# Performance work log

Measured on AMD Instinct MI355X. Metric: run time of the kernel, lower is better.

The kernel has to match this reference:

```python
import jax, jax.numpy as jnp
import numpy as np

DN = ('NCHW', 'OIHW', 'NCHW')

def conv(x, w, b=None, stride=1, pad=0):
    y = jax.lax.conv_general_dilated(x, w, (stride, stride), [(pad, pad), (pad, pad)],
                                     dimension_numbers=DN)
    return y if b is None else y + b[None, :, None, None]

def conv_t(x, w, b, stride=2, pad=1):
    # PyTorch ConvTranspose2d: w is (in, out, kh, kw); equivalent to an
    # input-dilated conv with spatially flipped, in/out-swapped kernel.
    k = w.shape[2]
    w2 = jnp.flip(w, (2, 3)).transpose(1, 0, 2, 3)
    p = k - 1 - pad
    y = jax.lax.conv_general_dilated(x, w2, (1, 1), [(p, p), (p, p)],
                                     lhs_dilation=(stride, stride), dimension_numbers=DN)
    return y + b[None, :, None, None]

def res_block(x, wa, wb):
    h = conv(jax.nn.relu(x), wa, None, 1, 1)   # 3x3, no bias
    h = conv(jax.nn.relu(h), wb, None, 1, 0)   # 1x1, no bias
    return x + h

def vq(x, codebook):
    B, C, H, W = x.shape
    xf = x.transpose(0, 2, 3, 1).reshape(-1, C)                      # (N, D)
    d = ((xf * xf).sum(-1, keepdims=True)
         - 2.0 * xf @ codebook.T
         + (codebook * codebook).sum(-1)[None, :])
    idx = jnp.argmin(d, axis=1)                                      # (N,)
    q = jnp.take(codebook, idx, axis=0)                              # gather (N, D)
    return q.reshape(B, H, W, C).transpose(0, 3, 1, 2)

def setup_inputs() -> dict:
    key = jax.random.key(0)
    ks = jax.random.split(key, 16)
    r = lambda i, shape: jax.random.normal(ks[i], shape, jnp.float32) * 0.05
    K, D = 512, 64
    return {
        'x': jax.random.normal(ks[0], (32, 1, 256, 256), jnp.float32),
        'w_e1': r(1, (32, 1, 4, 4)),   'b_e1': jnp.zeros((32,), jnp.float32),
        'w_e2': r(2, (64, 32, 4, 4)),  'b_e2': jnp.zeros((64,), jnp.float32),
        'w_er1a': r(3, (32, 64, 3, 3)), 'w_er1b': r(4, (64, 32, 1, 1)),
        'w_er2a': r(5, (32, 64, 3, 3)), 'w_er2b': r(6, (64, 32, 1, 1)),
        'w_pre': r(7, (D, 64, 1, 1)),  'b_pre': jnp.zeros((D,), jnp.float32),
        'codebook': jax.random.uniform(ks[8], (K, D), jnp.float32, -1.0 / K, 1.0 / K),
        'w_d1': r(9, (64, D, 3, 3)),   'b_d1': jnp.zeros((64,), jnp.float32),
        'w_dr1a': r(10, (32, 64, 3, 3)), 'w_dr1b': r(11, (64, 32, 1, 1)),
        'w_dr2a': r(12, (32, 64, 3, 3)), 'w_dr2b': r(13, (64, 32, 1, 1)),
        'w_t1': r(14, (64, 32, 4, 4)), 'b_t1': jnp.zeros((32,), jnp.float32),
        'w_t2': r(15, (32, 1, 4, 4)),  'b_t2': jnp.zeros((1,), jnp.float32),
    }

def reference(x, w_e1, b_e1, w_e2, b_e2, w_er1a, w_er1b, w_er2a, w_er2b,
              w_pre, b_pre, codebook, w_d1, b_d1, w_dr1a, w_dr1b,
              w_dr2a, w_dr2b, w_t1, b_t1, w_t2, b_t2):
    # Encoder
    h = jax.nn.relu(conv(x, w_e1, b_e1, 2, 1))     # (B,32,128,128)
    h = conv(h, w_e2, b_e2, 2, 1)                  # (B,64,64,64)
    h = res_block(h, w_er1a, w_er1b)
    h = res_block(h, w_er2a, w_er2b)
    # pre-VQ 1x1 conv
    h = conv(h, w_pre, b_pre, 1, 0)                # (B,64,64,64)
    # Vector quantization
    q = vq(h, codebook)
    # Decoder
    d = conv(q, w_d1, b_d1, 1, 1)
    d = res_block(d, w_dr1a, w_dr1b)
    d = res_block(d, w_dr2a, w_dr2b)
    d = jax.nn.relu(conv_t(d, w_t1, b_t1))         # (B,32,128,128)
    d = conv_t(d, w_t2, b_t2)                      # (B,1,256,256)
    return d
```

## Files before the change

kernel.cpp:

```cpp
#include <hip/hip_runtime.h>
#include <hip/hip_bf16.h>


__device__ __forceinline__ float rp_elem(const float* __restrict__ src,
                                         int i, int COUT, int CIN, int KK)
{
    const int co = i % COUT;
    const int t  = i / COUT;
    const int kk = t % KK;
    const int ci = t / KK;
    return src[(co * CIN + ci) * KK + kk];
}

__global__ __launch_bounds__(256) void repack_all(
    const float* __restrict__ e1,  const float* __restrict__ e2,
    const float* __restrict__ er1a, const float* __restrict__ er1b,
    const float* __restrict__ er2a, const float* __restrict__ er2b,
    const float* __restrict__ pre, const float* __restrict__ d1,
    const float* __restrict__ dr1a, const float* __restrict__ dr1b,
    const float* __restrict__ dr2a, const float* __restrict__ dr2b,
    const float* __restrict__ t1, const float* __restrict__ cb,
    float* __restrict__ WR)
{
    const int idx = blockIdx.x * 256 + threadIdx.x;
    if (idx >= 221696) return;
    float v;
    if      (idx < 512)    v = rp_elem(e1,   idx,          32,  1, 16);
    else if (idx < 33280)  v = rp_elem(e2,   idx - 512,    64, 32, 16);
    else if (idx < 51712)  v = rp_elem(er1a, idx - 33280,  32, 64,  9);
    else if (idx < 53760)  v = rp_elem(er1b, idx - 51712,  64, 32,  1);
    else if (idx < 72192)  v = rp_elem(er2a, idx - 53760,  32, 64,  9);
    else if (idx < 74240)  v = rp_elem(er2b, idx - 72192,  64, 32,  1);
    else if (idx < 78336)  v = rp_elem(pre,  idx - 74240,  64, 64,  1);
    else if (idx < 115200) v = rp_elem(d1,   idx - 78336,  64, 64,  9);
    else if (idx < 133632) v = rp_elem(dr1a, idx - 115200, 32, 64,  9);
    else if (idx < 135680) v = rp_elem(dr1b, idx - 133632, 64, 32,  1);
    else if (idx < 154112) v = rp_elem(dr2a, idx - 135680, 32, 64,  9);
    else if (idx < 156160) v = rp_elem(dr2b, idx - 154112, 64, 32,  1);
    else if (idx < 188928) {
        const int i  = idx - 156160;
        const int co = i & 31;
        const int q  = (i >> 5) & 3;
        const int k2 = (i >> 7) & 127;
        const int pr = i >> 14;
        const int pc = q >> 1, tb = q & 1;
        const int ci = k2 >> 1, ta = k2 & 1;
        const int kh = (1 - pr) + 2 * ta, kw = (1 - pc) + 2 * tb;
        v = t1[((ci * 32 + co) * 4 + kh) * 4 + kw];
    } else {
        const int i = idx - 188928;
        const int code = i & 511;
        const int dim  = i >> 9;
        v = cb[code * 64 + dim];
    }
    WR[idx] = v;
}

__global__ __launch_bounds__(256) void vq_prep_ee(
    const float* __restrict__ cb, float* __restrict__ ee)
{
    const int k = blockIdx.x * 256 + threadIdx.x;
    const float* __restrict__ cp = cb + (size_t)k * 64;
    float s = 0.0f;
#pragma unroll
    for (int i = 0; i < 64; i++) s = fmaf(cp[i], cp[i], s);
    ee[k] = s;
}

template<int CTOT, int CPB, int CIN, int K, int S, int PAD,
         bool RELU_IN, bool HAS_BIAS, bool RESID, bool RELU_OUT>
__global__ __launch_bounds__(256) void conv_gemm(
    const float* __restrict__ in, const float* __restrict__ wr,
    const float* __restrict__ bias, const float* __restrict__ resid,
    float* __restrict__ out,
    int H, int W, int OH, int OW)
{
    constexpr int KK  = K * K;
    constexpr int CIC = (K == 1) ? 8 : 1;
    constexpr int TS  = (K == 4) ? 2 : 1;
    constexpr int KC  = CIC * KK / TS;
    constexpr int NCH = (CIN * TS) / CIC;
    constexpr int NT  = 256;
    constexpr int CPTHD = CPB / 4;
    __shared__ __align__(16) float As[2][KC * NT];

    const int tid = threadIdx.x;
    const int tpx = tid & 63;
    const int tco = __builtin_amdgcn_readfirstlane(tid >> 6);
    const int co0 = blockIdx.y * CPB + tco * CPTHD;

    const int ohow = OH * OW;
    const int n_st = blockIdx.x * NT + tid;
    const int b_st = n_st / ohow;
    const int hw_s = n_st % ohow;
    const int ih0 = (hw_s / OW) * S - PAD;
    const int iw0 = (hw_s % OW) * S - PAD;
    const float* __restrict__ inb = in + (size_t)b_st * CIN * H * W;

    float acc[CPTHD][4];
#pragma unroll
    for (int c = 0; c < CPTHD; c++) {
        const float bz = HAS_BIAS ? bias[co0 + c] : 0.0f;
#pragma unroll
        for (int q = 0; q < 4; q++) acc[c][q] = bz;
    }

    float pf[KC];
    auto stage_load = [&](int ch) {
#pragma unroll
        for (int t = 0; t < KC; t++) {
            int ci, kh, kw;
            if constexpr (K == 1) {
                ci = ch * 8 + t; kh = 0; kw = 0;
            } else if constexpr (K == 3) {
                ci = ch; kh = t / 3; kw = t % 3;
            } else {
                ci = ch >> 1;
                const int kk = ((ch & 1) << 3) + t;
                kh = kk >> 2; kw = kk & 3;
            }
            const int ih = ih0 + kh, iw = iw0 + kw;
            float v = 0.0f;
            if (ih >= 0 && ih < H && iw >= 0 && iw < W)
                v = inb[(size_t)ci * H * W + ih * W + iw];
            if (RELU_IN) v = fmaxf(v, 0.0f);
            pf[t] = v;
        }
    };

    stage_load(0);
#pragma unroll
    for (int t = 0; t < KC; t++) As[0][t * NT + tid] = pf[t];
    __syncthreads();

#pragma unroll 2
    for (int c = 0; c < NCH; c++) {
        const int cur = c & 1;
        if (c + 1 < NCH) stage_load(c + 1);

#pragma unroll
        for (int t = 0; t < KC; t++) {
            const float4 a4 = *(const float4*)(As[cur] + t * NT + tpx * 4);
            const float* __restrict__ wk =
                wr + (size_t)(c * KC + t) * CTOT + co0;
#pragma unroll
            for (int cc = 0; cc < CPTHD; cc++) {
                const float w = wk[cc];
                acc[cc][0] = fmaf(a4.x, w, acc[cc][0]);
                acc[cc][1] = fmaf(a4.y, w, acc[cc][1]);
                acc[cc][2] = fmaf(a4.z, w, acc[cc][2]);
                acc[cc][3] = fmaf(a4.w, w, acc[cc][3]);
            }
        }

        if (c + 1 < NCH) {
#pragma unroll
            for (int t = 0; t < KC; t++) As[1 - cur][t * NT + tid] = pf[t];
        }
        __syncthreads();
    }

    const int n_c  = blockIdx.x * NT + tpx * 4;
    const int b_c  = n_c / ohow;
    const int hw_c = n_c % ohow;
    float* __restrict__ op = out + (size_t)b_c * CTOT * ohow + hw_c;
    const float* __restrict__ rp =
        RESID ? (resid + (size_t)b_c * CTOT * ohow + hw_c) : nullptr;
#pragma unroll
    for (int c = 0; c < CPTHD; c++) {
        const size_t off = (size_t)(co0 + c) * ohow;
        float4 r = make_float4(acc[c][0], acc[c][1], acc[c][2], acc[c][3]);
        if (RESID) {
            const float4 rv = *(const float4*)(rp + off);
            r.x += rv.x; r.y += rv.y; r.z += rv.z; r.w += rv.w;
        }
        if (RELU_OUT) {
            r.x = fmaxf(r.x, 0.f); r.y = fmaxf(r.y, 0.f);
            r.z = fmaxf(r.z, 0.f); r.w = fmaxf(r.w, 0.f);
        }
        *(float4*)(op + off) = r;
    }
}

__global__ __launch_bounds__(512, 4) void res_tile(
    const float* __restrict__ in, const float* __restrict__ wr1,
    const float* __restrict__ wr2, float* __restrict__ out)
{
    __shared__ __align__(16) float S[13824];

    const int tid = threadIdx.x;
    const int p   = tid & 127;
    const int cog = __builtin_amdgcn_readfirstlane(tid >> 7);
    const int a   = p >> 5;
    const int c0  = (p & 31) * 2;

    const int n0   = blockIdx.x * 256;
    const int b    = n0 >> 12;
    const int row0 = (n0 & 4095) >> 6;
    const float* __restrict__ inb = in + (size_t)b * 64 * 4096;

    float4 pf4[7];
    auto stage_issue = [&](int half) {
#pragma unroll
        for (int m = 0; m < 7; m++) {
            const int f4 = m * 512 + tid;
            float4 v = make_float4(0.f, 0.f, 0.f, 0.f);
            if (f4 < 3456) {
                const int ci  = f4 / 108;
                const int rem = f4 - ci * 108;
                const int r6  = rem / 18;
                const int c4  = rem - r6 * 18;
                const int ih  = row0 + r6 - 1;
                if (ih >= 0 && ih < 64 && c4 >= 1 && c4 <= 16)
                    v = *(const float4*)(inb + (size_t)(half * 32 + ci) * 4096
                                         + ih * 64 + (c4 * 4 - 4));
            }
            pf4[m] = v;
        }
    };
    auto stage_commit = [&]() {
#pragma unroll
        for (int m = 0; m < 7; m++) {
            const int f4 = m * 512 + tid;
            if (f4 < 3456) {
                float4 v = pf4[m];
                v.x = fmaxf(v.x, 0.f); v.y = fmaxf(v.y, 0.f);
                v.z = fmaxf(v.z, 0.f); v.w = fmaxf(v.w, 0.f);
                *(float4*)(S + f4 * 4) = v;
            }
        }
    };

    const int co1 = cog * 8;
    float acc1[8][2];
#pragma unroll
    for (int c = 0; c < 8; c++) { acc1[c][0] = 0.0f; acc1[c][1] = 0.0f; }

    auto conv1_half = [&](int h) {
#pragma unroll 2
        for (int c = 0; c < 32; c++) {
            const float* __restrict__ wb =
                wr1 + (size_t)((h * 32 + c) * 9) * 32 + co1;
#pragma unroll
            for (int kh = 0; kh < 3; kh++) {
                const float* __restrict__ tp =
                    S + c * 432 + (a + kh) * 72 + 4 + c0;
                const float2 L = *(const float2*)(tp - 2);
                const float2 M = *(const float2*)(tp);
                const float2 R = *(const float2*)(tp + 2);
                const float xm = L.y;
                const float x0 = M.x;
                const float x1 = M.y;
                const float x2 = R.x;
                const float* __restrict__ wk = wb + (size_t)(kh * 3) * 32;
#pragma unroll
                for (int cc = 0; cc < 8; cc++) {
                    const float w = wk[cc];
                    acc1[cc][0] = fmaf(xm, w, acc1[cc][0]);
                    acc1[cc][1] = fmaf(x0, w, acc1[cc][1]);
                }
#pragma unroll
                for (int cc = 0; cc < 8; cc++) {
                    const float w = wk[32 + cc];
                    acc1[cc][0] = fmaf(x0, w, acc1[cc][0]);
                    acc1[cc][1] = fmaf(x1, w, acc1[cc][1]);
                }
#pragma unroll
                for (int cc = 0; cc < 8; cc++) {
                    const float w = wk[64 + cc];
                    acc1[cc][0] = fmaf(x1, w, acc1[cc][0]);
                    acc1[cc][1] = fmaf(x2, w, acc1[cc][1]);
                }
            }
        }
    };

    stage_issue(0);
    stage_commit();
    __syncthreads();
    stage_issue(1);
    conv1_half(0);
    __syncthreads();
    stage_commit();
    __syncthreads();
    conv1_half(1);
    __syncthreads();

#pragma unroll
    for (int cc = 0; cc < 8; cc++)
        *(float2*)(S + (co1 + cc) * 256 + p * 2) =
            make_float2(acc1[cc][0], acc1[cc][1]);
    __syncthreads();

    const int co2 = cog * 16;
    float acc2[16][2];
#pragma unroll
    for (int c = 0; c < 16; c++) { acc2[c][0] = 0.0f; acc2[c][1] = 0.0f; }

#pragma unroll 4
    for (int k = 0; k < 32; k++) {
        float2 m2 = *(const float2*)(S + k * 256 + p * 2);
        m2.x = fmaxf(m2.x, 0.f);
        m2.y = fmaxf(m2.y, 0.f);
        const float* __restrict__ wk = wr2 + (size_t)k * 64 + co2;
#pragma unroll
        for (int cc = 0; cc < 16; cc++) {
            const float w = wk[cc];
            acc2[cc][0] = fmaf(m2.x, w, acc2[cc][0]);
            acc2[cc][1] = fmaf(m2.y, w, acc2[cc][1]);
        }
    }

    const int hw = (n0 & 4095) + p * 2;
    const float* __restrict__ rp = inb + hw;
    float* __restrict__ op = out + (size_t)b * 64 * 4096 + hw;
#pragma unroll
    for (int cc = 0; cc < 16; cc++) {
        const size_t off = (size_t)(co2 + cc) * 4096;
        const float2 rv = *(const float2*)(rp + off);
        *(float2*)(op + off) =
            make_float2(acc2[cc][0] + rv.x, acc2[cc][1] + rv.y);
    }
}

__global__ __launch_bounds__(512, 4) void conv3_tile(
    const float* __restrict__ in, const float* __restrict__ wr,
    const float* __restrict__ bias, float* __restrict__ out)
{
    __shared__ __align__(16) float S[13824];

    const int tid = threadIdx.x;
    const int p   = tid & 127;
    const int cog = __builtin_amdgcn_readfirstlane(tid >> 7);
    const int a   = p >> 5;
    const int c0  = (p & 31) * 2;

    const int n0   = blockIdx.x * 256;
    const int b    = n0 >> 12;
    const int row0 = (n0 & 4095) >> 6;
    const float* __restrict__ inb = in + (size_t)b * 64 * 4096;

    float4 pf4[7];
    auto stage_issue = [&](int half) {
#pragma unroll
        for (int m = 0; m < 7; m++) {
            const int f4 = m * 512 + tid;
            float4 v = make_float4(0.f, 0.f, 0.f, 0.f);
            if (f4 < 3456) {
                const int ci  = f4 / 108;
                const int rem = f4 - ci * 108;
                const int r6  = rem / 18;
                const int c4  = rem - r6 * 18;
                const int ih  = row0 + r6 - 1;
                if (ih >= 0 && ih < 64 && c4 >= 1 && c4 <= 16)
                    v = *(const float4*)(inb + (size_t)(half * 32 + ci) * 4096
                                         + ih * 64 + (c4 * 4 - 4));
            }
            pf4[m] = v;
        }
    };
    auto stage_commit = [&]() {
#pragma unroll
        for (int m = 0; m < 7; m++) {
            const int f4 = m * 512 + tid;
            if (f4 < 3456) *(float4*)(S + f4 * 4) = pf4[m];
        }
    };

    const int co1 = cog * 16;
    float acc[16][2];
#pragma unroll
    for (int cc = 0; cc < 16; cc++) {
        const float bz = bias[co1 + cc];
        acc[cc][0] = bz; acc[cc][1] = bz;
    }

    auto conv_half = [&](int h) {
#pragma unroll 2
        for (int c = 0; c < 32; c++) {
            const float* __restrict__ wb =
                wr + (size_t)((h * 32 + c) * 9) * 64 + co1;
#pragma unroll
            for (int kh = 0; kh < 3; kh++) {
                const float* __restrict__ tp =
                    S + c * 432 + (a + kh) * 72 + 4 + c0;
                const float2 L = *(const float2*)(tp - 2);
                const float2 M = *(const float2*)(tp);
                const float2 R = *(const float2*)(tp + 2);
                const float xm = L.y;
                const float x0 = M.x;
                const float x1 = M.y;
                const float x2 = R.x;
                const float* __restrict__ wk = wb + (size_t)(kh * 3) * 64;
#pragma unroll
                for (int cc = 0; cc < 16; cc++) {
                    const float w = wk[cc];
                    acc[cc][0] = fmaf(xm, w, acc[cc][0]);
                    acc[cc][1] = fmaf(x0, w, acc[cc][1]);
                }
#pragma unroll
                for (int cc = 0; cc < 16; cc++) {
                    const float w = wk[64 + cc];
                    acc[cc][0] = fmaf(x0, w, acc[cc][0]);
                    acc[cc][1] = fmaf(x1, w, acc[cc][1]);
                }
#pragma unroll
                for (int cc = 0; cc < 16; cc++) {
                    const float w = wk[128 + cc];
                    acc[cc][0] = fmaf(x1, w, acc[cc][0]);
                    acc[cc][1] = fmaf(x2, w, acc[cc][1]);
                }
            }
        }
    };

    stage_issue(0);
    stage_commit();
    __syncthreads();
    stage_issue(1);
    conv_half(0);
    __syncthreads();
    stage_commit();
    __syncthreads();
    conv_half(1);

    const int hw = (n0 & 4095) + p * 2;
    float* __restrict__ op = out + (size_t)b * 64 * 4096 + hw;
#pragma unroll
    for (int cc = 0; cc < 16; cc++)
        *(float2*)(op + (size_t)(co1 + cc) * 4096) =
            make_float2(acc[cc][0], acc[cc][1]);
}

__global__ __launch_bounds__(512, 4) void conv4s2_tile(
    const float* __restrict__ in, const float* __restrict__ wr,
    const float* __restrict__ bias, float* __restrict__ out)
{
    __shared__ __align__(16) float S[13056];

    const int tid = threadIdx.x;
    const int p   = tid & 63;
    const int cog = __builtin_amdgcn_readfirstlane(tid >> 6);
    const int a   = p >> 5;
    const int c0  = (p & 31) * 2;

    const int n0   = blockIdx.x * 128;
    const int b    = n0 >> 12;
    const int row0 = (n0 & 4095) >> 6;
    const float* __restrict__ inb = in + (size_t)b * 32 * 16384;

    float4 pf4[7];
    auto stage_issue = [&](int half) {
#pragma unroll
        for (int m = 0; m < 7; m++) {
            const int f4 = m * 512 + tid;
            float4 v = make_float4(0.f, 0.f, 0.f, 0.f);
            if (f4 < 3264) {
                const int ci  = f4 / 204;
                const int rem = f4 - ci * 204;
                const int r6  = rem / 34;
                const int s   = rem - r6 * 34;
                const int ih  = 2 * row0 - 1 + r6;
                if (ih >= 0 && ih < 128 && s >= 1 && s <= 32)
                    v = *(const float4*)(inb + (size_t)(half * 16 + ci) * 16384
                                         + ih * 128 + (s - 1) * 4);
            }
            pf4[m] = v;
        }
    };
    auto stage_commit = [&]() {
#pragma unroll
        for (int m = 0; m < 7; m++) {
            const int f4 = m * 512 + tid;
            if (f4 < 3264) *(float4*)(S + f4 * 4) = pf4[m];
        }
    };

    const int co1 = cog * 8;
    float acc[8][2];
#pragma unroll
    for (int cc = 0; cc < 8; cc++) {
        const float bz = bias[co1 + cc];
        acc[cc][0] = bz; acc[cc][1] = bz;
    }

    auto conv_half = [&](int h) {
#pragma unroll 2
        for (int c = 0; c < 16; c++) {
            const float* __restrict__ wb =
                wr + (size_t)((h * 16 + c) * 16) * 64 + co1;
#pragma unroll
            for (int kh = 0; kh < 4; kh++) {
                const float* __restrict__ base =
                    S + c * 816 + (2 * a + kh) * 136 + 2 * c0;
                const float4 Q = *(const float4*)(base + 4);
                const float x0 = base[3];
                const float x5 = base[8];
                const float x1 = Q.x, x2 = Q.y, x3 = Q.z, x4 = Q.w;
                const float* __restrict__ wk = wb + (size_t)(kh * 4) * 64;
#pragma unroll
                for (int cc = 0; cc < 8; cc++) {
                    const float w = wk[cc];
                    acc[cc][0] = fmaf(x0, w, acc[cc][0]);
                    acc[cc][1] = fmaf(x2, w, acc[cc][1]);
                }
#pragma unroll
                for (int cc = 0; cc < 8; cc++) {
                    const float w = wk[64 + cc];
                    acc[cc][0] = fmaf(x1, w, acc[cc][0]);
                    acc[cc][1] = fmaf(x3, w, acc[cc][1]);
                }
#pragma unroll
                for (int cc = 0; cc < 8; cc++) {
                    const float w = wk[128 + cc];
                    acc[cc][0] = fmaf(x2, w, acc[cc][0]);
                    acc[cc][1] = fmaf(x4, w, acc[cc][1]);
                }
#pragma unroll
                for (int cc = 0; cc < 8; cc++) {
                    const float w = wk[192 + cc];
                    acc[cc][0] = fmaf(x3, w, acc[cc][0]);
                    acc[cc][1] = fmaf(x5, w, acc[cc][1]);
                }
            }
        }
    };

    stage_issue(0);
    stage_commit();
    __syncthreads();
    stage_issue(1);
    conv_half(0);
    __syncthreads();
    stage_commit();
    __syncthreads();
    conv_half(1);

    const int hw = (n0 & 4095) + p * 2;
    float* __restrict__ op = out + (size_t)b * 64 * 4096 + hw;
#pragma unroll
    for (int cc = 0; cc < 8; cc++)
        *(float2*)(op + (size_t)(co1 + cc) * 4096) =
            make_float2(acc[cc][0], acc[cc][1]);
}

__global__ __launch_bounds__(512, 4) void conv1x1_tile(
    const float* __restrict__ in, const float* __restrict__ wr,
    const float* __restrict__ bias, float* __restrict__ out)
{
    __shared__ __align__(16) float S[8192];

    const int tid = threadIdx.x;
    const int p   = tid & 127;
    const int cog = __builtin_amdgcn_readfirstlane(tid >> 7);

    const int n0  = blockIdx.x * 256;
    const int b   = n0 >> 12;
    const int hw0 = n0 & 4095;
    const float* __restrict__ inb = in + (size_t)b * 64 * 4096 + hw0;

    float4 pf4[4];
    auto stage_issue = [&](int half) {
#pragma unroll
        for (int m = 0; m < 4; m++) {
            const int f4 = m * 512 + tid;
            const int ci = f4 >> 6;
            const int c4 = f4 & 63;
            pf4[m] = *(const float4*)(inb + (size_t)(half * 32 + ci) * 4096
                                      + c4 * 4);
        }
    };
    auto stage_commit = [&]() {
#pragma unroll
        for (int m = 0; m < 4; m++) {
            const int f4 = m * 512 + tid;
            *(float4*)(S + f4 * 4) = pf4[m];
        }
    };

    const int co1 = cog * 16;
    float acc[16][2];
#pragma unroll
    for (int cc = 0; cc < 16; cc++) {
        const float bz = bias[co1 + cc];
        acc[cc][0] = bz; acc[cc][1] = bz;
    }

    auto conv_half = [&](int h) {
#pragma unroll 4
        for (int c = 0; c < 32; c++) {
            const float2 x = *(const float2*)(S + c * 256 + p * 2);
            const float* __restrict__ wk =
                wr + (size_t)(h * 32 + c) * 64 + co1;
#pragma unroll
            for (int cc = 0; cc < 16; cc++) {
                const float w = wk[cc];
                acc[cc][0] = fmaf(x.x, w, acc[cc][0]);
                acc[cc][1] = fmaf(x.y, w, acc[cc][1]);
            }
        }
    };

    stage_issue(0);
    stage_commit();
    __syncthreads();
    stage_issue(1);
    conv_half(0);
    __syncthreads();
    stage_commit();
    __syncthreads();
    conv_half(1);

    float* __restrict__ op = out + (size_t)b * 64 * 4096 + hw0 + p * 2;
#pragma unroll
    for (int cc = 0; cc < 16; cc++)
        *(float2*)(op + (size_t)(co1 + cc) * 4096) =
            make_float2(acc[cc][0], acc[cc][1]);
}

__global__ __launch_bounds__(512, 4) void convt_tile(
    const float* __restrict__ in, const float* __restrict__ wr,
    const float* __restrict__ bias, float* __restrict__ out)
{
    __shared__ __align__(16) float S[13824];

    const int tid = threadIdx.x;
    const int p   = tid & 127;
    const int cog = __builtin_amdgcn_readfirstlane(tid >> 7);
    const int a   = p >> 5;
    const int c0  = (p & 31) * 2;

    const int n0   = blockIdx.x * 256;
    const int b    = n0 >> 12;
    const int row0 = (n0 & 4095) >> 6;
    const float* __restrict__ inb = in + (size_t)b * 64 * 4096;

    float4 pf4[7];
    auto stage_issue = [&](int half) {
#pragma unroll
        for (int m = 0; m < 7; m++) {
            const int f4 = m * 512 + tid;
            float4 v = make_float4(0.f, 0.f, 0.f, 0.f);
            if (f4 < 3456) {
                const int ci  = f4 / 108;
                const int rem = f4 - ci * 108;
                const int r6  = rem / 18;
                const int c4  = rem - r6 * 18;
                const int ih  = row0 + r6 - 1;
                if (ih >= 0 && ih < 64 && c4 >= 1 && c4 <= 16)
                    v = *(const float4*)(inb + (size_t)(half * 32 + ci) * 4096
                                         + ih * 64 + (c4 * 4 - 4));
            }
            pf4[m] = v;
        }
    };
    auto stage_commit = [&]() {
#pragma unroll
        for (int m = 0; m < 7; m++) {
            const int f4 = m * 512 + tid;
            if (f4 < 3456) *(float4*)(S + f4 * 4) = pf4[m];
        }
    };

    const int co1 = cog * 8;
    float acc[8][2][2][2];
#pragma unroll
    for (int cc = 0; cc < 8; cc++) {
        const float bz = bias[co1 + cc];
#pragma unroll
        for (int px = 0; px < 2; px++)
#pragma unroll
            for (int pc = 0; pc < 2; pc++) {
                acc[cc][px][pc][0] = bz;
                acc[cc][px][pc][1] = bz;
            }
    }

    auto conv_half = [&](int h) {
#pragma unroll 2
        for (int c = 0; c < 32; c++) {
            const int ci = h * 32 + c;
            float X[3][4];
#pragma unroll
            for (int r = 0; r < 3; r++) {
                const float* __restrict__ tp =
                    S + c * 432 + (a + r) * 72 + 4 + c0;
                const float2 L = *(const float2*)(tp - 2);
                const float2 M = *(const float2*)(tp);
                const float2 R = *(const float2*)(tp + 2);
                X[r][0] = L.y; X[r][1] = M.x; X[r][2] = M.y; X[r][3] = R.x;
            }
            const float* __restrict__ wb = wr + (size_t)(ci * 2) * 128 + co1;
#pragma unroll
            for (int ta = 0; ta < 2; ta++) {
                const float* X0 = X[1 - ta];
                const float* X1 = X[2 - ta];
                const float* __restrict__ wt = wb + ta * 128;
#pragma unroll
                for (int tb = 0; tb < 2; tb++) {
#pragma unroll
                    for (int pc = 0; pc < 2; pc++) {
                        const int m = pc - tb + 1;
                        const float* __restrict__ w0 = wt + (pc * 2 + tb) * 32;
                        const float* __restrict__ w1 = w0 + 16384;
#pragma unroll
                        for (int cc = 0; cc < 8; cc++) {
                            const float wv0 = w0[cc];
                            const float wv1 = w1[cc];
                            acc[cc][0][pc][0] =
                                fmaf(X0[m],     wv0, acc[cc][0][pc][0]);
                            acc[cc][1][pc][0] =
                                fmaf(X0[m + 1], wv0, acc[cc][1][pc][0]);
                            acc[cc][0][pc][1] =
                                fmaf(X1[m],     wv1, acc[cc][0][pc][1]);
                            acc[cc][1][pc][1] =
                                fmaf(X1[m + 1], wv1, acc[cc][1][pc][1]);
                        }
                    }
                }
            }
        }
    };

    stage_issue(0);
    stage_commit();
    __syncthreads();
    stage_issue(1);
    conv_half(0);
    __syncthreads();
    stage_commit();
    __syncthreads();
    conv_half(1);

    const int i = row0 + a;
    float* __restrict__ ob =
        out + (size_t)b * 32 * 16384 + (size_t)(2 * i) * 128 + 2 * c0;
#pragma unroll
    for (int cc = 0; cc < 8; cc++) {
        float* __restrict__ o = ob + (size_t)(co1 + cc) * 16384;
#pragma unroll
        for (int pr = 0; pr < 2; pr++) {
            const float4 v = make_float4(
                fmaxf(acc[cc][0][0][pr], 0.f), fmaxf(acc[cc][0][1][pr], 0.f),
                fmaxf(acc[cc][1][0][pr], 0.f), fmaxf(acc[cc][1][1][pr], 0.f));
            *(float4*)(o + (size_t)pr * 128) = v;
        }
    }
}

__global__ __launch_bounds__(256) void convt2_quad(
    const float* __restrict__ in, const float* __restrict__ w,
    const float* __restrict__ bias, float* __restrict__ out, int B)
{
    const int IH = 128, IW = 128, CIN = 32, OW = 256;
    const int j = threadIdx.x & 127;
    const int i = (blockIdx.x << 1) + (threadIdx.x >> 7);
    const int b = blockIdx.y;

    const float* __restrict__ inb = in + (size_t)b * CIN * IH * IW;
    const float bz = bias[0];
    float a00 = bz, a01 = bz, a10 = bz, a11 = bz;

    const bool okm = (i > 0);
    const bool okp = (i < IH - 1);
    const bool olm = (j > 0);
    const bool olp = (j < IW - 1);

#pragma unroll 4
    for (int ci = 0; ci < CIN; ci++) {
        const float* __restrict__ p = inb + ((size_t)ci * IH + i) * IW + j;
        const float* __restrict__ wp = w + ci * 16;
        const float vmm = (okm && olm) ? p[-IW - 1] : 0.f;
        const float vm0 = okm ? p[-IW] : 0.f;
        const float vmp = (okm && olp) ? p[-IW + 1] : 0.f;
        const float v0m = olm ? p[-1] : 0.f;
        const float v00 = p[0];
        const float v0p = olp ? p[1] : 0.f;
        const float vpm = (okp && olm) ? p[IW - 1] : 0.f;
        const float vp0 = okp ? p[IW] : 0.f;
        const float vpp = (okp && olp) ? p[IW + 1] : 0.f;
        a00 = fmaf(v00, wp[1 * 4 + 1], a00);
        a00 = fmaf(v0m, wp[1 * 4 + 3], a00);
        a00 = fmaf(vm0, wp[3 * 4 + 1], a00);
        a00 = fmaf(vmm, wp[3 * 4 + 3], a00);
        a01 = fmaf(v0p, wp[1 * 4 + 0], a01);
        a01 = fmaf(v00, wp[1 * 4 + 2], a01);
        a01 = fmaf(vmp, wp[3 * 4 + 0], a01);
        a01 = fmaf(vm0, wp[3 * 4 + 2], a01);
        a10 = fmaf(vp0, wp[0 * 4 + 1], a10);
        a10 = fmaf(vpm, wp[0 * 4 + 3], a10);
        a10 = fmaf(v00, wp[2 * 4 + 1], a10);
        a10 = fmaf(v0m, wp[2 * 4 + 3], a10);
        a11 = fmaf(vpp, wp[0 * 4 + 0], a11);
        a11 = fmaf(vp0, wp[0 * 4 + 2], a11);
        a11 = fmaf(v0p, wp[2 * 4 + 0], a11);
        a11 = fmaf(v00, wp[2 * 4 + 2], a11);
    }

    float* __restrict__ outb = out + (size_t)b * 256 * 256;
    ((float2*)(outb + (size_t)(2 * i) * OW))[j] = make_float2(a00, a01);
    ((float2*)(outb + (size_t)(2 * i + 1) * OW))[j] = make_float2(a10, a11);
}

__global__ __launch_bounds__(256) void vq_gemm(
    const float* __restrict__ h,
    const float* __restrict__ cb,
    const float* __restrict__ cbT,
    const float* __restrict__ ee,
    float* __restrict__ q)
{
    __shared__ __align__(16) float As[64 * 128];
    __shared__ float xx_sh[128];
    __shared__ float pd[4 * 128];
    __shared__ int   pk[4 * 128];
    __shared__ int   bidx_sh[128];

    const int tid = threadIdx.x;
    const int tpx = tid & 63;
    const int w = __builtin_amdgcn_readfirstlane(tid >> 6);
    const int n0 = blockIdx.x * 128;
    const int b  = n0 >> 12;
    const int hw0 = n0 & 4095;

    const float* __restrict__ hb = h + (size_t)b * 64 * 4096 + hw0;
#pragma unroll
    for (int m = 0; m < 32; m++) {
        const int idx = m * 256 + tid;
        const int k = idx >> 7, p = idx & 127;
        As[idx] = hb[(size_t)k * 4096 + p];
    }
    __syncthreads();

    if (tid < 128) {
        float s = 0.0f;
#pragma unroll
        for (int i = 0; i < 64; i++) {
            const float v = As[i * 128 + tid];
            s = fmaf(v, v, s);
        }
        xx_sh[tid] = s;
    }
    __syncthreads();

    const float xx0 = xx_sh[tpx * 2];
    const float xx1 = xx_sh[tpx * 2 + 1];
    const int cwave = w * 128;

    float best0 = 3.402823466e+38f, best1 = 3.402823466e+38f;
    int bk0 = 0, bk1 = 0;

#pragma unroll 1
    for (int ch = 0; ch < 16; ch++) {
        const int cbase = cwave + ch * 8;
        float acc[8][2];
#pragma unroll
        for (int c = 0; c < 8; c++) { acc[c][0] = 0.0f; acc[c][1] = 0.0f; }

#pragma unroll 8
        for (int k = 0; k < 64; k++) {
            const float2 a2 = *(const float2*)(As + k * 128 + tpx * 2);
            const float* __restrict__ wk = cbT + (size_t)k * 512 + cbase;
#pragma unroll
            for (int c = 0; c < 8; c++) {
                const float wv = wk[c];
                acc[c][0] = fmaf(a2.x, wv, acc[c][0]);
                acc[c][1] = fmaf(a2.y, wv, acc[c][1]);
            }
        }
        const float* __restrict__ eep = ee + cbase;
#pragma unroll
        for (int c = 0; c < 8; c++) {
            const float eec = eep[c];
            const float d0 = xx0 - 2.0f * acc[c][0] + eec;
            const float d1 = xx1 - 2.0f * acc[c][1] + eec;
            if (d0 < best0) { best0 = d0; bk0 = cbase + c; }
            if (d1 < best1) { best1 = d1; bk1 = cbase + c; }
        }
    }

    pd[w * 128 + tpx * 2]     = best0;
    pd[w * 128 + tpx * 2 + 1] = best1;
    pk[w * 128 + tpx * 2]     = bk0;
    pk[w * 128 + tpx * 2 + 1] = bk1;
    __syncthreads();

    if (tid < 128) {
        float bd = pd[tid]; int bk = pk[tid];
#pragma unroll
        for (int ww = 1; ww < 4; ww++) {
            const float od = pd[ww * 128 + tid];
            if (od < bd) { bd = od; bk = pk[ww * 128 + tid]; }
        }
        bidx_sh[tid] = bk;
    }
    __syncthreads();

    {
        const int p  = tid & 127;
        const int d0 = (tid >> 7) * 32;
        const int bk = bidx_sh[p];
        const float4* __restrict__ cp4 = (const float4*)(cb + (size_t)bk * 64 + d0);
        float* __restrict__ qb = q + ((size_t)b * 64 + d0) * 4096 + hw0 + p;
#pragma unroll
        for (int i = 0; i < 8; i++) {
            const float4 v = cp4[i];
            qb[(size_t)(4 * i + 0) * 4096] = v.x;
            qb[(size_t)(4 * i + 1) * 4096] = v.y;
            qb[(size_t)(4 * i + 2) * 4096] = v.z;
            qb[(size_t)(4 * i + 3) * 4096] = v.w;
        }
    }
}

extern "C" void kernel_launch(void* const* d_in, const int* in_sizes, int n_in,
                              void* d_out, int out_size, void* d_ws, size_t ws_size,
                              hipStream_t stream) {
    const float* x      = (const float*)d_in[0];
    const float* w_e1   = (const float*)d_in[1];
    const float* b_e1   = (const float*)d_in[2];
    const float* w_e2   = (const float*)d_in[3];
    const float* b_e2   = (const float*)d_in[4];
    const float* w_er1a = (const float*)d_in[5];
    const float* w_er1b = (const float*)d_in[6];
    const float* w_er2a = (const float*)d_in[7];
    const float* w_er2b = (const float*)d_in[8];
    const float* w_pre  = (const float*)d_in[9];
    const float* b_pre  = (const float*)d_in[10];
    const float* cbk    = (const float*)d_in[11];
    const float* w_d1   = (const float*)d_in[12];
    const float* b_d1   = (const float*)d_in[13];
    const float* w_dr1a = (const float*)d_in[14];
    const float* w_dr1b = (const float*)d_in[15];
    const float* w_dr2a = (const float*)d_in[16];
    const float* w_dr2b = (const float*)d_in[17];
    const float* w_t1   = (const float*)d_in[18];
    const float* b_t1   = (const float*)d_in[19];
    const float* w_t2   = (const float*)d_in[20];
    const float* b_t2   = (const float*)d_in[21];
    float* out = (float*)d_out;

    float* A  = (float*)d_ws;
    float* Bb = A  + 16777216;
    float* C  = Bb + 8388608;
    float* D  = C  + 4194304;
    float* WR = D  + 8388608;
    float* EE = WR + 221696;

    float* r_e1  = WR;
    float* r_e2  = WR + 512;
    float* r_er1a = WR + 33280;
    float* r_er1b = WR + 51712;
    float* r_er2a = WR + 53760;
    float* r_er2b = WR + 72192;
    float* r_pre = WR + 74240;
    float* r_d1  = WR + 78336;
    float* r_dr1a = WR + 115200;
    float* r_dr1b = WR + 133632;
    float* r_dr2a = WR + 135680;
    float* r_dr2b = WR + 154112;
    float* r_t1  = WR + 156160;
    float* r_cbT = WR + 188928;

    const dim3 blk(256);
    const dim3 blk512(512);

    repack_all<<<dim3(866), blk, 0, stream>>>(
        w_e1, w_e2, w_er1a, w_er1b, w_er2a, w_er2b, w_pre, w_d1,
        w_dr1a, w_dr1b, w_dr2a, w_dr2b, w_t1, cbk, WR);
    vq_prep_ee<<<dim3(2), blk, 0, stream>>>(cbk, EE);

    conv_gemm<32, 32, 1, 4, 2, 1, false, true, false, true>
        <<<dim3(2048, 1), blk, 0, stream>>>(x, r_e1, b_e1, nullptr, A,
                                            256, 256, 128, 128);
    conv4s2_tile<<<dim3(1024), blk512, 0, stream>>>(A, r_e2, b_e2, Bb);
    res_tile<<<dim3(512), blk512, 0, stream>>>(Bb, r_er1a, r_er1b, A);
    res_tile<<<dim3(512), blk512, 0, stream>>>(A, r_er2a, r_er2b, Bb);
    conv1x1_tile<<<dim3(512), blk512, 0, stream>>>(Bb, r_pre, b_pre, D);
    vq_gemm<<<dim3(1024), blk, 0, stream>>>(D, cbk, r_cbT, EE, Bb);
    conv3_tile<<<dim3(512), blk512, 0, stream>>>(Bb, r_d1, b_d1, D);
    res_tile<<<dim3(512), blk512, 0, stream>>>(D, r_dr1a, r_dr1b, A);
    res_tile<<<dim3(512), blk512, 0, stream>>>(A, r_dr2a, r_dr2b, D);
    convt_tile<<<dim3(512), blk512, 0, stream>>>(D, r_t1, b_t1, A);
    convt2_quad<<<dim3(64, 32), blk, 0, stream>>>(A, w_t2, b_t2, out, 32);
}
```

Before: 895.8 us.

## Deinterleave conv4s2 shared tile into even/odd columns and remap threads

The stride-2 4x4 conv kernel now stores each staged input row split into even and odd column halves in shared memory, so each thread reads four scalar values with unit-stride, conflict-free addressing instead of a float4 plus strided scalars. Thread mapping changes from 64 pixels x 8 channel groups (2 outputs x 8 channels per thread) to 128 pixels x 4 channel groups (1 output x 16 channels per thread). This aims to cut LDS bank conflicts and improve weight reuse per load. In exchange the commit step does more address arithmetic and output stores become scalar rather than float2.

```diff
diff --git a/kernel.cpp b/kernel.cpp
--- a/kernel.cpp
+++ b/kernel.cpp
@@ -439,10 +439,10 @@
     __shared__ __align__(16) float S[13056];
 
     const int tid = threadIdx.x;
-    const int p   = tid & 63;
-    const int cog = __builtin_amdgcn_readfirstlane(tid >> 6);
-    const int a   = p >> 5;
-    const int c0  = (p & 31) * 2;
+    const int p   = tid & 127;
+    const int cog = __builtin_amdgcn_readfirstlane(tid >> 7);
+    const int a   = p >> 6;
+    const int j   = p & 63;
 
     const int n0   = blockIdx.x * 128;
     const int b    = n0 >> 12;
@@ -472,17 +472,23 @@
 #pragma unroll
         for (int m = 0; m < 7; m++) {
             const int f4 = m * 512 + tid;
-            if (f4 < 3264) *(float4*)(S + f4 * 4) = pf4[m];
-        }
-    };
-
-    const int co1 = cog * 8;
-    float acc[8][2];
-#pragma unroll
-    for (int cc = 0; cc < 8; cc++) {
-        const float bz = bias[co1 + cc];
-        acc[cc][0] = bz; acc[cc][1] = bz;
-    }
+            if (f4 < 3264) {
+                const int ci  = f4 / 204;
+                const int rem = f4 - ci * 204;
+                const int r6  = rem / 34;
+                const int s   = rem - r6 * 34;
+                const float4 v = pf4[m];
+                float* __restrict__ rowp = S + (ci * 6 + r6) * 136;
+                *(float2*)(rowp + 2 * s)      = make_float2(v.x, v.z);
+                *(float2*)(rowp + 68 + 2 * s) = make_float2(v.y, v.w);
+            }
+        }
+    };
+
+    const int co1 = cog * 16;
+    float acc[16];
+#pragma unroll
+    for (int cc = 0; cc < 16; cc++) acc[cc] = bias[co1 + cc];
 
     auto conv_half = [&](int h) {
 #pragma unroll 2
@@ -491,37 +497,25 @@
                 wr + (size_t)((h * 16 + c) * 16) * 64 + co1;
 #pragma unroll
             for (int kh = 0; kh < 4; kh++) {
-                const float* __restrict__ base =
-                    S + c * 816 + (2 * a + kh) * 136 + 2 * c0;
-                const float4 Q = *(const float4*)(base + 4);
-                const float x0 = base[3];
-                const float x5 = base[8];
-                const float x1 = Q.x, x2 = Q.y, x3 = Q.z, x4 = Q.w;
+                const float* __restrict__ rowp =
+                    S + (c * 6 + 2 * a + kh) * 136;
+                const float e0 = rowp[j + 2];
+                const float e1 = rowp[j + 3];
+                const float o0 = rowp[68 + j + 1];
+                const float o1 = rowp[68 + j + 2];
                 const float* __restrict__ wk = wb + (size_t)(kh * 4) * 64;
 #pragma unroll
-                for (int cc = 0; cc < 8; cc++) {
-                    const float w = wk[cc];
-                    acc[cc][0] = fmaf(x0, w, acc[cc][0]);
-                    acc[cc][1] = fmaf(x2, w, acc[cc][1]);
-                }
-#pragma unroll
-                for (int cc = 0; cc < 8; cc++) {
-                    const float w = wk[64 + cc];
-                    acc[cc][0] = fmaf(x1, w, acc[cc][0]);
-                    acc[cc][1] = fmaf(x3, w, acc[cc][1]);
-                }
-#pragma unroll
-                for (int cc = 0; cc < 8; cc++) {
-                    const float w = wk[128 + cc];
-                    acc[cc][0] = fmaf(x2, w, acc[cc][0]);
-                    acc[cc][1] = fmaf(x4, w, acc[cc][1]);
-                }
-#pragma unroll
-                for (int cc = 0; cc < 8; cc++) {
-                    const float w = wk[192 + cc];
-                    acc[cc][0] = fmaf(x3, w, acc[cc][0]);
-                    acc[cc][1] = fmaf(x5, w, acc[cc][1]);
-                }
+                for (int cc = 0; cc < 16; cc++)
+                    acc[cc] = fmaf(o0, wk[cc], acc[cc]);
+#pragma unroll
+                for (int cc = 0; cc < 16; cc++)
+                    acc[cc] = fmaf(e0, wk[64 + cc], acc[cc]);
+#pragma unroll
+                for (int cc = 0; cc < 16; cc++)
+                    acc[cc] = fmaf(o1, wk[128 + cc], acc[cc]);
+#pragma unroll
+                for (int cc = 0; cc < 16; cc++)
+                    acc[cc] = fmaf(e1, wk[192 + cc], acc[cc]);
             }
         }
     };
@@ -536,12 +530,11 @@
     __syncthreads();
     conv_half(1);
 
-    const int hw = (n0 & 4095) + p * 2;
+    const int hw = (n0 & 4095) + a * 64 + j;
     float* __restrict__ op = out + (size_t)b * 64 * 4096 + hw;
 #pragma unroll
-    for (int cc = 0; cc < 8; cc++)
-        *(float2*)(op + (size_t)(co1 + cc) * 4096) =
-            make_float2(acc[cc][0], acc[cc][1]);
+    for (int cc = 0; cc < 16; cc++)
+        op[(size_t)(co1 + cc) * 4096] = acc[cc];
 }
 
 __global__ __launch_bounds__(512, 4) void conv1x1_tile(
```

Result: no change. 904.0 us (+0.9%).
